# Kernel optimization log

Measured on AMD Instinct MI355X. Metric: run time of the kernel, lower is better.

Reference implementation:

```python
import jax, jax.numpy as jnp
import numpy as np

N, E, D, H, C = 50000, 800000, 64, 2, 64  # nodes, edges, feat, heads, per-head out


def _transformer_conv(x, src, dst, wq, bq, wk, bk, wv, bv, ws, bs):
    n = x.shape[0]
    q = (x @ wq + bq).reshape(n, H, C)
    k = (x @ wk + bk).reshape(n, H, C)
    v = (x @ wv + bv).reshape(n, H, C)
    qi = q[dst]           # [E,H,C] gather at target nodes
    kj = k[src]           # [E,H,C] gather at source nodes
    vj = v[src]
    alpha = jnp.einsum('ehc,ehc->eh', qi, kj) / jnp.sqrt(jnp.asarray(C, x.dtype))
    # segment softmax over incoming edges of each dst node
    amax = jax.ops.segment_max(alpha, dst, num_segments=n)          # [N,H]
    amax = jnp.where(jnp.isfinite(amax), amax, 0.0)
    ex = jnp.exp(alpha - amax[dst])                                  # [E,H]
    denom = jax.ops.segment_sum(ex, dst, num_segments=n)            # [N,H]
    a = ex / (denom[dst] + 1e-16)
    out = jax.ops.segment_sum(a[:, :, None] * vj, dst, num_segments=n)  # [N,H,C]
    out = out.mean(axis=1)                                           # concat=False -> mean heads
    return out + x @ ws + bs                                         # root (skip) connection


def setup_inputs() -> dict:
    key = jax.random.key(0)
    ks = jax.random.split(key, 20)
    x = jax.random.normal(ks[0], (N, D), dtype=jnp.float32)
    edge_index = jax.random.randint(ks[1], (2, E), 0, N, dtype=jnp.int64)
    s = 1.0 / np.sqrt(D)
    def lin(k, din, dout):
        return jax.random.uniform(k, (din, dout), jnp.float32, -s, s)
    inp = {"x": x, "edge_index": edge_index}
    i = 2
    for l, din in ((1, D), (2, C)):
        for nm, dout in (("wq", H * C), ("wk", H * C), ("wv", H * C), ("ws", C)):
            inp[f"l{l}_{nm}"] = lin(ks[i], din, dout); i += 1
            inp[f"l{l}_{nm.replace('w','b')}"] = jnp.zeros((dout,), jnp.float32)
    return inp


def reference(x, edge_index,
              l1_wq, l1_bq, l1_wk, l1_bk, l1_wv, l1_bv, l1_ws, l1_bs,
              l2_wq, l2_bq, l2_wk, l2_bk, l2_wv, l2_bv, l2_ws, l2_bs):
    src, dst = edge_index[0], edge_index[1]
    h = _transformer_conv(x, src, dst, l1_wq, l1_bq, l1_wk, l1_bk, l1_wv, l1_bv, l1_ws, l1_bs)
    h = _transformer_conv(h, src, dst, l2_wq, l2_bq, l2_wk, l2_bk, l2_wv, l2_bv, l2_ws, l2_bs)
    return h
```

## Files before the change

### kernel.cpp

```cpp
#include <hip/hip_runtime.h>
#include <hip/hip_fp16.h>
#include <math.h>


typedef _Float16 half8 __attribute__((ext_vector_type(8)));
typedef _Float16 half4 __attribute__((ext_vector_type(4)));
typedef float floatx4 __attribute__((ext_vector_type(4)));

struct __align__(16) H8 { __half2 a, b, c, d; };
struct __align__(16) F16x8 { _Float16 v[8]; };

static __device__ inline __half2 shfl_xor_h2(__half2 v, int off) {
    union { __half2 h; int i; } u;
    u.h = v;
    u.i = __shfl_xor(u.i, off);
    return u.h;
}

__global__ __launch_bounds__(256) void prep_w_both(
    const float* __restrict__ W0, const float* __restrict__ B0,
    const float* __restrict__ W1, const float* __restrict__ B1,
    const float* __restrict__ W2, const float* __restrict__ B2,
    const float* __restrict__ W3, const float* __restrict__ B3,
    const float* __restrict__ W4, const float* __restrict__ B4,
    const float* __restrict__ W5, const float* __restrict__ B5,
    const float* __restrict__ W6, const float* __restrict__ B6,
    const float* __restrict__ W7, const float* __restrict__ B7,
    _Float16* __restrict__ wht1, _Float16* __restrict__ wht2,
    float* __restrict__ ball1, float* __restrict__ ball2,
    int* __restrict__ counts, int n) {
    const int tid = blockIdx.x * 256 + threadIdx.x;
    const int nt  = gridDim.x * 256;
    for (int idx = tid; idx < 448 * 64; idx += nt) {
        int c = idx >> 6, k = idx & 63;
        float v1, v2;
        if (c < 128)      { v1 = W0[k*128 + c];       v2 = W4[k*128 + c]; }
        else if (c < 256) { v1 = W1[k*128 + (c-128)]; v2 = W5[k*128 + (c-128)]; }
        else if (c < 384) { v1 = W2[k*128 + (c-256)]; v2 = W6[k*128 + (c-256)]; }
        else              { v1 = W3[k*64 + (c-384)];  v2 = W7[k*64 + (c-384)]; }
        wht1[c*64 + k] = (_Float16)v1;
        wht2[c*64 + k] = (_Float16)v2;
        if (k == 0) {
            float b1, b2;
            if (c < 128)      { b1 = B0[c];     b2 = B4[c]; }
            else if (c < 256) { b1 = B1[c-128]; b2 = B5[c-128]; }
            else if (c < 384) { b1 = B2[c-256]; b2 = B6[c-256]; }
            else              { b1 = B3[c-384]; b2 = B7[c-384]; }
            ball1[c] = b1;
            ball2[c] = b2;
        }
    }
    for (int i = tid; i < n; i += nt) counts[i] = 0;
}

__global__ __launch_bounds__(256) void hist_kernel(const int* __restrict__ dst,
                                                   int* __restrict__ counts, int e) {
    int i = blockIdx.x * 256 + threadIdx.x;
    if (i < e) atomicAdd(&counts[dst[i]], 1);
}

__global__ __launch_bounds__(256) void partial_kernel(const int* __restrict__ counts,
                                                      int* __restrict__ partials, int n) {
    int idx = blockIdx.x * 256 + threadIdx.x;
    int v = (idx < n) ? counts[idx] : 0;
    for (int off = 1; off < 64; off <<= 1) v += __shfl_xor(v, off);
    __shared__ int ws[4];
    int wid = threadIdx.x >> 6;
    if ((threadIdx.x & 63) == 0) ws[wid] = v;
    __syncthreads();
    if (threadIdx.x == 0) partials[blockIdx.x] = ws[0] + ws[1] + ws[2] + ws[3];
}

__global__ __launch_bounds__(256) void scanp_kernel(const int* __restrict__ partials,
                                                    int* __restrict__ blockbase, int nb) {
    __shared__ int s[256];
    int t = threadIdx.x;
    int v = (t < nb) ? partials[t] : 0;
    s[t] = v;
    __syncthreads();
    for (int off = 1; off < 256; off <<= 1) {
        int u = (t >= off) ? s[t - off] : 0;
        __syncthreads();
        s[t] += u;
        __syncthreads();
    }
    if (t < nb) blockbase[t] = s[t] - v;
}

__global__ __launch_bounds__(256) void final_kernel(const int* __restrict__ counts,
                                                    const int* __restrict__ blockbase,
                                                    int* __restrict__ offsets,
                                                    int* __restrict__ cursor,
                                                    int n, int total) {
    __shared__ int s[256];
    int t = threadIdx.x;
    int idx = blockIdx.x * 256 + t;
    int v = (idx < n) ? counts[idx] : 0;
    s[t] = v;
    __syncthreads();
    for (int off = 1; off < 256; off <<= 1) {
        int u = (t >= off) ? s[t - off] : 0;
        __syncthreads();
        s[t] += u;
        __syncthreads();
    }
    if (idx < n) {
        int ex = blockbase[blockIdx.x] + s[t] - v;
        offsets[idx] = ex;
        cursor[idx]  = ex;
    }
    if (idx == 0) offsets[n] = total;
}

__global__ __launch_bounds__(256) void scatter_kernel(const int* __restrict__ src,
                                                      const int* __restrict__ dst,
                                                      int* __restrict__ cursor,
                                                      int* __restrict__ ssrc, int e) {
    int i = blockIdx.x * 256 + threadIdx.x;
    if (i < e) {
        int pos = atomicAdd(&cursor[dst[i]], 1);
        ssrc[pos] = src[i];
    }
}

template <int F32IN>
__global__ __launch_bounds__(256) void gemm_mfma(
    const void* __restrict__ Xin, int rows,
    const _Float16* __restrict__ WhT,
    const float* __restrict__ Ball,
    _Float16* __restrict__ Qo,
    _Float16* __restrict__ KVo,
    float* __restrict__ So) {
    const int lane = threadIdx.x & 63;
    const int w    = threadIdx.x >> 6;
    const int kg   = lane >> 4;
    const int li   = lane & 15;
    const int rbase = blockIdx.x * 64 + w * 16;
    const int row  = rbase + li;
    const int crow = row < rows ? row : rows - 1;

    half8 a0, a1;
    if constexpr (F32IN) {
        const float* xp = (const float*)Xin + (size_t)crow * 64 + kg * 8;
        float4 f0 = *(const float4*)xp;
        float4 f1 = *(const float4*)(xp + 4);
        float4 f2 = *(const float4*)(xp + 32);
        float4 f3 = *(const float4*)(xp + 36);
        a0 = half8{(_Float16)f0.x, (_Float16)f0.y, (_Float16)f0.z, (_Float16)f0.w,
                   (_Float16)f1.x, (_Float16)f1.y, (_Float16)f1.z, (_Float16)f1.w};
        a1 = half8{(_Float16)f2.x, (_Float16)f2.y, (_Float16)f2.z, (_Float16)f2.w,
                   (_Float16)f3.x, (_Float16)f3.y, (_Float16)f3.z, (_Float16)f3.w};
    } else {
        const _Float16* xp = (const _Float16*)Xin + (size_t)crow * 64 + kg * 8;
        a0 = *(const half8*)xp;
        a1 = *(const half8*)(xp + 32);
    }

#pragma unroll
    for (int t = 0; t < 28; ++t) {
        const _Float16* wp = WhT + (size_t)(t * 16 + li) * 64 + kg * 8;
        half8 b0 = *(const half8*)wp;
        half8 b1 = *(const half8*)(wp + 32);
        floatx4 acc = {0.f, 0.f, 0.f, 0.f};
        acc = __builtin_amdgcn_mfma_f32_16x16x32_f16(b0, a0, acc, 0, 0, 0);
        acc = __builtin_amdgcn_mfma_f32_16x16x32_f16(b1, a1, acc, 0, 0, 0);
        const int c0 = t * 16 + kg * 4;
        float4 bias = *(const float4*)(Ball + c0);
        if (row < rows) {
            float o0 = acc[0] + bias.x, o1 = acc[1] + bias.y;
            float o2 = acc[2] + bias.z, o3 = acc[3] + bias.w;
            if (t < 8) {
                *(half4*)(Qo + (size_t)row * 128 + c0) =
                    half4{(_Float16)o0, (_Float16)o1, (_Float16)o2, (_Float16)o3};
            } else if (t < 24) {
                *(half4*)(KVo + (size_t)row * 256 + (c0 - 128)) =
                    half4{(_Float16)o0, (_Float16)o1, (_Float16)o2, (_Float16)o3};
            } else {
                *(float4*)(So + (size_t)row * 64 + (c0 - 384)) =
                    make_float4(o0, o1, o2, o3);
            }
        }
    }
}

template <int HALF_OUT>
__global__ __launch_bounds__(256) void attn_kernel(
    const _Float16* __restrict__ Qh,
    const _Float16* __restrict__ KV,
    const int* __restrict__ offs, const int* __restrict__ ssrc,
    const float* __restrict__ skip,
    float* __restrict__ outF, _Float16* __restrict__ outH, int n) {
    int node = (blockIdx.x * 256 + threadIdx.x) >> 6;
    int lane = threadIdx.x & 63;
    if (node >= n) return;
    const int slot = lane >> 4;
    const int koff = ((lane >> 3) & 1) * 64 + (lane & 7) * 8;

    H8 q = *(const H8*)(Qh + (size_t)node * 128 + koff);

    const int beg = offs[node], end = offs[node + 1];
    float m = -INFINITY, l = 0.f;
    __half2 hz = __float2half2_rn(0.f);
    __half2 ha = hz, hb = hz, hc = hz, hd = hz;

    int i = beg;
    bool b0 = false, b1 = false;
    H8 k0, k1, v0, v1;
    if (i < end) {
        int e0 = i + slot, e1 = i + 4 + slot;
        b0 = e0 < end; b1 = e1 < end;
        int s0 = ssrc[b0 ? e0 : end - 1];
        int s1 = ssrc[b1 ? e1 : end - 1];
        const _Float16* p0 = KV + (size_t)s0 * 256 + koff;
        const _Float16* p1 = KV + (size_t)s1 * 256 + koff;
        k0 = *(const H8*)p0; v0 = *(const H8*)(p0 + 128);
        k1 = *(const H8*)p1; v1 = *(const H8*)(p1 + 128);
    }

    while (i < end) {
        const int inext = i + 8;
        bool nb0 = false, nb1 = false;
        H8 nk0, nk1, nv0, nv1;
        if (inext < end) {
            int e0 = inext + slot, e1 = inext + 4 + slot;
            nb0 = e0 < end; nb1 = e1 < end;
            int s0 = ssrc[nb0 ? e0 : end - 1];
            int s1 = ssrc[nb1 ? e1 : end - 1];
            const _Float16* p0 = KV + (size_t)s0 * 256 + koff;
            const _Float16* p1 = KV + (size_t)s1 * 256 + koff;
            nk0 = *(const H8*)p0; nv0 = *(const H8*)(p0 + 128);
            nk1 = *(const H8*)p1; nv1 = *(const H8*)(p1 + 128);
        }

        __half2 dh0 = __hfma2(q.a, k0.a, __hfma2(q.b, k0.b, __hfma2(q.c, k0.c, __hmul2(q.d, k0.d))));
        __half2 dh1 = __hfma2(q.a, k1.a, __hfma2(q.b, k1.b, __hfma2(q.c, k1.c, __hmul2(q.d, k1.d))));
        __half2 pd = __halves2half2(__hadd(dh0.x, dh0.y), __hadd(dh1.x, dh1.y));
        pd = __hadd2(pd, shfl_xor_h2(pd, 1));
        pd = __hadd2(pd, shfl_xor_h2(pd, 2));
        pd = __hadd2(pd, shfl_xor_h2(pd, 4));
        float d0 = b0 ? __half2float(pd.x) * 0.125f : -INFINITY;
        float d1 = b1 ? __half2float(pd.y) * 0.125f : -INFINITY;

        float mx = fmaxf(fmaxf(d0, d1), m);
        float sc = (m == -INFINITY) ? 0.f : __expf(m - mx);
        float p0e = b0 ? __expf(d0 - mx) : 0.f;
        float p1e = b1 ? __expf(d1 - mx) : 0.f;
        l = fmaf(l, sc, p0e + p1e);

        __half2 hsc = __float2half2_rn(sc);
        __half2 hp0 = __float2half2_rn(p0e);
        __half2 hp1 = __float2half2_rn(p1e);
        ha = __hfma2(hp0, v0.a, __hfma2(hp1, v1.a, __hmul2(ha, hsc)));
        hb = __hfma2(hp0, v0.b, __hfma2(hp1, v1.b, __hmul2(hb, hsc)));
        hc = __hfma2(hp0, v0.c, __hfma2(hp1, v1.c, __hmul2(hc, hsc)));
        hd = __hfma2(hp0, v0.d, __hfma2(hp1, v1.d, __hmul2(hd, hsc)));
        m = mx;

        i = inext;
        b0 = nb0; b1 = nb1;
        k0 = nk0; k1 = nk1; v0 = nv0; v1 = nv1;
    }

    float acc[8];
    {
        float2 t0 = __half22float2(ha), t1 = __half22float2(hb);
        float2 t2 = __half22float2(hc), t3 = __half22float2(hd);
        acc[0] = t0.x; acc[1] = t0.y; acc[2] = t1.x; acc[3] = t1.y;
        acc[4] = t2.x; acc[5] = t2.y; acc[6] = t3.x; acc[7] = t3.y;
    }

#pragma unroll
    for (int off = 16; off <= 32; off <<= 1) {
        float mo = __shfl_xor(m, off);
        float lo = __shfl_xor(l, off);
        float ao[8];
#pragma unroll
        for (int j = 0; j < 8; ++j) ao[j] = __shfl_xor(acc[j], off);
        float mm = fmaxf(m, mo);
        float sa = (m  == -INFINITY) ? 0.f : __expf(m  - mm);
        float sb = (mo == -INFINITY) ? 0.f : __expf(mo - mm);
        l = l * sa + lo * sb;
#pragma unroll
        for (int j = 0; j < 8; ++j) acc[j] = acc[j] * sa + ao[j] * sb;
        m = mm;
    }
    float inv = 1.f / (l + 1e-16f);
    float r[8];
#pragma unroll
    for (int j = 0; j < 8; ++j) r[j] = acc[j] * inv;
#pragma unroll
    for (int j = 0; j < 8; ++j) r[j] = 0.5f * (r[j] + __shfl_xor(r[j], 8));

    if (lane < 8) {
        const float4* sp = (const float4*)(skip + (size_t)node * 64 + lane * 8);
        float4 s0 = sp[0], s1 = sp[1];
        float o[8] = {s0.x + r[0], s0.y + r[1], s0.z + r[2], s0.w + r[3],
                      s1.x + r[4], s1.y + r[5], s1.z + r[6], s1.w + r[7]};
        if (HALF_OUT) {
            F16x8 h;
#pragma unroll
            for (int j = 0; j < 8; ++j) h.v[j] = (_Float16)o[j];
            *(F16x8*)(outH + (size_t)node * 64 + lane * 8) = h;
        } else {
            float4* op = (float4*)(outF + (size_t)node * 64 + lane * 8);
            op[0] = make_float4(o[0], o[1], o[2], o[3]);
            op[1] = make_float4(o[4], o[5], o[6], o[7]);
        }
    }
}

extern "C" void kernel_launch(void* const* d_in, const int* in_sizes, int n_in,
                              void* d_out, int out_size, void* d_ws, size_t ws_size,
                              hipStream_t stream) {
    const float* x  = (const float*)d_in[0];
    const int*   ei = (const int*)d_in[1];
    const int N = in_sizes[0] / 64;
    const int E = in_sizes[1] / 2;

    const float* w[16];
    for (int i = 0; i < 16; ++i) w[i] = (const float*)d_in[2 + i];

    char* base = (char*)d_ws;
    size_t off = 0;
    auto alloc = [&](size_t bytes) {
        void* p = base + off;
        off = (off + bytes + 255) & ~(size_t)255;
        return p;
    };
    _Float16* qh   = (_Float16*)alloc((size_t)N * 128 * 2);
    _Float16* kv   = (_Float16*)alloc((size_t)N * 256 * 2);
    float*    sk1  = (float*)alloc((size_t)N * 64 * 4);
    _Float16* h1h  = (_Float16*)alloc((size_t)N * 64 * 2);
    _Float16* wht1 = (_Float16*)alloc(448 * 64 * 2);
    _Float16* wht2 = (_Float16*)alloc(448 * 64 * 2);
    float*    ball1 = (float*)alloc(448 * 4);
    float*    ball2 = (float*)alloc(448 * 4);
    int* counts    = (int*)alloc((size_t)N * 4);
    int* offsets   = (int*)alloc((size_t)(N + 1) * 4);
    int* cursor    = (int*)alloc((size_t)N * 4);
    int* ssrc      = (int*)alloc((size_t)E * 4);
    int* partials  = (int*)alloc(1024 * 4);
    int* blockbase = (int*)alloc(1024 * 4);

    prep_w_both<<<224, 256, 0, stream>>>(
        w[0], w[1], w[2], w[3], w[4], w[5], w[6], w[7],
        w[8], w[9], w[10], w[11], w[12], w[13], w[14], w[15],
        wht1, wht2, ball1, ball2, counts, N);

    int eb = (E + 255) / 256;
    int nb = (N + 255) / 256;
    hist_kernel<<<eb, 256, 0, stream>>>(ei + E, counts, E);
    partial_kernel<<<nb, 256, 0, stream>>>(counts, partials, N);
    scanp_kernel<<<1, 256, 0, stream>>>(partials, blockbase, nb);
    final_kernel<<<nb, 256, 0, stream>>>(counts, blockbase, offsets, cursor, N, E);
    scatter_kernel<<<eb, 256, 0, stream>>>(ei, ei + E, cursor, ssrc, E);

    const int gb = (N + 63) / 64;
    const int ab = (N * 64 + 255) / 256;

    gemm_mfma<1><<<gb, 256, 0, stream>>>(x, N, wht1, ball1, qh, kv, sk1);
    attn_kernel<1><<<ab, 256, 0, stream>>>(qh, kv, offsets, ssrc, sk1,
                                           nullptr, h1h, N);
    gemm_mfma<0><<<gb, 256, 0, stream>>>(h1h, N, wht2, ball2, qh, kv, (float*)d_out);
    attn_kernel<0><<<ab, 256, 0, stream>>>(qh, kv, offsets, ssrc, (float*)d_out,
                                           (float*)d_out, nullptr, N);
}
```

Baseline: 281.0 us.

## Fuse CSR build and first-layer GEMM into one cooperative kernel

Replaces the chain of weight prep, histogram, partial sums, scans, scatter and the layer-1 GEMM with a single cooperative kernel of 1024 blocks that uses grid-wide syncs between phases. The layer-1 GEMM tiles run in the same phase as the degree histogram so the two overlap. The aim is to remove several kernel launch gaps and tail effects from small kernels. The old multi-kernel path is kept as a fallback if the cooperative launch fails. In exchange it adds grid.sync costs and depends on 1024 blocks being co-resident.

```diff
diff --git a/kernel.cpp b/kernel.cpp
--- a/kernel.cpp
+++ b/kernel.cpp
@@ -1,5 +1,6 @@
 #include <hip/hip_runtime.h>
 #include <hip/hip_fp16.h>
+#include <hip/hip_cooperative_groups.h>
 #include <math.h>
 
 
@@ -17,125 +18,17 @@
     return u.h;
 }
 
-__global__ __launch_bounds__(256) void prep_w_both(
-    const float* __restrict__ W0, const float* __restrict__ B0,
-    const float* __restrict__ W1, const float* __restrict__ B1,
-    const float* __restrict__ W2, const float* __restrict__ B2,
-    const float* __restrict__ W3, const float* __restrict__ B3,
-    const float* __restrict__ W4, const float* __restrict__ B4,
-    const float* __restrict__ W5, const float* __restrict__ B5,
-    const float* __restrict__ W6, const float* __restrict__ B6,
-    const float* __restrict__ W7, const float* __restrict__ B7,
-    _Float16* __restrict__ wht1, _Float16* __restrict__ wht2,
-    float* __restrict__ ball1, float* __restrict__ ball2,
-    int* __restrict__ counts, int n) {
-    const int tid = blockIdx.x * 256 + threadIdx.x;
-    const int nt  = gridDim.x * 256;
-    for (int idx = tid; idx < 448 * 64; idx += nt) {
-        int c = idx >> 6, k = idx & 63;
-        float v1, v2;
-        if (c < 128)      { v1 = W0[k*128 + c];       v2 = W4[k*128 + c]; }
-        else if (c < 256) { v1 = W1[k*128 + (c-128)]; v2 = W5[k*128 + (c-128)]; }
-        else if (c < 384) { v1 = W2[k*128 + (c-256)]; v2 = W6[k*128 + (c-256)]; }
-        else              { v1 = W3[k*64 + (c-384)];  v2 = W7[k*64 + (c-384)]; }
-        wht1[c*64 + k] = (_Float16)v1;
-        wht2[c*64 + k] = (_Float16)v2;
-        if (k == 0) {
-            float b1, b2;
-            if (c < 128)      { b1 = B0[c];     b2 = B4[c]; }
-            else if (c < 256) { b1 = B1[c-128]; b2 = B5[c-128]; }
-            else if (c < 384) { b1 = B2[c-256]; b2 = B6[c-256]; }
-            else              { b1 = B3[c-384]; b2 = B7[c-384]; }
-            ball1[c] = b1;
-            ball2[c] = b2;
-        }
-    }
-    for (int i = tid; i < n; i += nt) counts[i] = 0;
-}
-
-__global__ __launch_bounds__(256) void hist_kernel(const int* __restrict__ dst,
-                                                   int* __restrict__ counts, int e) {
-    int i = blockIdx.x * 256 + threadIdx.x;
-    if (i < e) atomicAdd(&counts[dst[i]], 1);
-}
-
-__global__ __launch_bounds__(256) void partial_kernel(const int* __restrict__ counts,
-                                                      int* __restrict__ partials, int n) {
-    int idx = blockIdx.x * 256 + threadIdx.x;
-    int v = (idx < n) ? counts[idx] : 0;
-    for (int off = 1; off < 64; off <<= 1) v += __shfl_xor(v, off);
-    __shared__ int ws[4];
-    int wid = threadIdx.x >> 6;
-    if ((threadIdx.x & 63) == 0) ws[wid] = v;
-    __syncthreads();
-    if (threadIdx.x == 0) partials[blockIdx.x] = ws[0] + ws[1] + ws[2] + ws[3];
-}
-
-__global__ __launch_bounds__(256) void scanp_kernel(const int* __restrict__ partials,
-                                                    int* __restrict__ blockbase, int nb) {
-    __shared__ int s[256];
-    int t = threadIdx.x;
-    int v = (t < nb) ? partials[t] : 0;
-    s[t] = v;
-    __syncthreads();
-    for (int off = 1; off < 256; off <<= 1) {
-        int u = (t >= off) ? s[t - off] : 0;
-        __syncthreads();
-        s[t] += u;
-        __syncthreads();
-    }
-    if (t < nb) blockbase[t] = s[t] - v;
-}
-
-__global__ __launch_bounds__(256) void final_kernel(const int* __restrict__ counts,
-                                                    const int* __restrict__ blockbase,
-                                                    int* __restrict__ offsets,
-                                                    int* __restrict__ cursor,
-                                                    int n, int total) {
-    __shared__ int s[256];
-    int t = threadIdx.x;
-    int idx = blockIdx.x * 256 + t;
-    int v = (idx < n) ? counts[idx] : 0;
-    s[t] = v;
-    __syncthreads();
-    for (int off = 1; off < 256; off <<= 1) {
-        int u = (t >= off) ? s[t - off] : 0;
-        __syncthreads();
-        s[t] += u;
-        __syncthreads();
-    }
-    if (idx < n) {
-        int ex = blockbase[blockIdx.x] + s[t] - v;
-        offsets[idx] = ex;
-        cursor[idx]  = ex;
-    }
-    if (idx == 0) offsets[n] = total;
-}
-
-__global__ __launch_bounds__(256) void scatter_kernel(const int* __restrict__ src,
-                                                      const int* __restrict__ dst,
-                                                      int* __restrict__ cursor,
-                                                      int* __restrict__ ssrc, int e) {
-    int i = blockIdx.x * 256 + threadIdx.x;
-    if (i < e) {
-        int pos = atomicAdd(&cursor[dst[i]], 1);
-        ssrc[pos] = src[i];
-    }
-}
-
 template <int F32IN>
-__global__ __launch_bounds__(256) void gemm_mfma(
+static __device__ __forceinline__ void gemm_tile_body(
     const void* __restrict__ Xin, int rows,
-    const _Float16* __restrict__ WhT,
-    const float* __restrict__ Ball,
-    _Float16* __restrict__ Qo,
-    _Float16* __restrict__ KVo,
-    float* __restrict__ So) {
-    const int lane = threadIdx.x & 63;
-    const int w    = threadIdx.x >> 6;
+    const _Float16* __restrict__ WhT, const float* __restrict__ Ball,
+    _Float16* __restrict__ Qo, _Float16* __restrict__ KVo,
+    float* __restrict__ So, int blk, int tix) {
+    const int lane = tix & 63;
+    const int w    = tix >> 6;
     const int kg   = lane >> 4;
     const int li   = lane & 15;
-    const int rbase = blockIdx.x * 64 + w * 16;
+    const int rbase = blk * 64 + w * 16;
     const int row  = rbase + li;
     const int crow = row < rows ? row : rows - 1;
 
@@ -183,6 +76,229 @@
     }
 }
 
+static __device__ __forceinline__ void prep_body(
+    const float* const* W, _Float16* wht1, _Float16* wht2,
+    float* ball1, float* ball2, int* counts, int n, int tid, int nt) {
+    for (int idx = tid; idx < 448 * 64; idx += nt) {
+        int c = idx >> 6, k = idx & 63;
+        float v1, v2;
+        if (c < 128)      { v1 = W[0][k*128 + c];        v2 = W[8][k*128 + c]; }
+        else if (c < 256) { v1 = W[2][k*128 + (c-128)];  v2 = W[10][k*128 + (c-128)]; }
+        else if (c < 384) { v1 = W[4][k*128 + (c-256)];  v2 = W[12][k*128 + (c-256)]; }
+        else              { v1 = W[6][k*64 + (c-384)];   v2 = W[14][k*64 + (c-384)]; }
+        wht1[c*64 + k] = (_Float16)v1;
+        wht2[c*64 + k] = (_Float16)v2;
+        if (k == 0) {
+            float b1, b2;
+            if (c < 128)      { b1 = W[1][c];       b2 = W[9][c]; }
+            else if (c < 256) { b1 = W[3][c-128];   b2 = W[11][c-128]; }
+            else if (c < 384) { b1 = W[5][c-256];   b2 = W[13][c-256]; }
+            else              { b1 = W[7][c-384];   b2 = W[15][c-384]; }
+            ball1[c] = b1;
+            ball2[c] = b2;
+        }
+    }
+    for (int i = tid; i < n; i += nt) counts[i] = 0;
+}
+
+struct SetupArgs {
+    const float* W[16];
+    const float* x;
+    const int* ei;
+    int* counts;
+    int* offsets;
+    int* cursor;
+    int* ssrc;
+    int* partials;
+    int* blockbase;
+    _Float16* wht1;
+    _Float16* wht2;
+    float* ball1;
+    float* ball2;
+    _Float16* qh;
+    _Float16* kv;
+    float* sk1;
+    int N, E;
+};
+
+__global__ __launch_bounds__(256, 4) void setup_coop(SetupArgs a) {
+    namespace cg = cooperative_groups;
+    cg::grid_group grid = cg::this_grid();
+    const int tid = blockIdx.x * 256 + threadIdx.x;
+    const int nt  = gridDim.x * 256;
+    __shared__ int sh[256];
+    __shared__ int ws[4];
+
+    prep_body(a.W, a.wht1, a.wht2, a.ball1, a.ball2, a.counts, a.N, tid, nt);
+    grid.sync();
+
+    {
+        const int ntile = (a.N + 63) >> 6;
+        for (int tb = blockIdx.x; tb < ntile; tb += gridDim.x)
+            gemm_tile_body<1>(a.x, a.N, a.wht1, a.ball1, a.qh, a.kv, a.sk1,
+                              tb, threadIdx.x);
+        const int* dst = a.ei + a.E;
+        for (int i = tid; i < a.E; i += nt) atomicAdd(&a.counts[dst[i]], 1);
+    }
+    grid.sync();
+
+    const int nch = (a.N + 255) >> 8;
+    for (int b = blockIdx.x; b < nch; b += gridDim.x) {
+        int idx = b * 256 + threadIdx.x;
+        int v = (idx < a.N) ? a.counts[idx] : 0;
+        for (int off = 1; off < 64; off <<= 1) v += __shfl_xor(v, off);
+        if ((threadIdx.x & 63) == 0) ws[threadIdx.x >> 6] = v;
+        __syncthreads();
+        if (threadIdx.x == 0)
+            a.partials[b] = ws[0] + ws[1] + ws[2] + ws[3];
+        __syncthreads();
+    }
+    grid.sync();
+
+    if (blockIdx.x == 0) {
+        int t = threadIdx.x;
+        int v = (t < nch) ? a.partials[t] : 0;
+        sh[t] = v;
+        __syncthreads();
+        for (int off = 1; off < 256; off <<= 1) {
+            int u = (t >= off) ? sh[t - off] : 0;
+            __syncthreads();
+            sh[t] += u;
+            __syncthreads();
+        }
+        if (t < nch) a.blockbase[t] = sh[t] - v;
+    }
+    grid.sync();
+
+    for (int b = blockIdx.x; b < nch; b += gridDim.x) {
+        int t = threadIdx.x;
+        int idx = b * 256 + t;
+        int v = (idx < a.N) ? a.counts[idx] : 0;
+        sh[t] = v;
+        __syncthreads();
+        for (int off = 1; off < 256; off <<= 1) {
+            int u = (t >= off) ? sh[t - off] : 0;
+            __syncthreads();
+            sh[t] += u;
+            __syncthreads();
+        }
+        if (idx < a.N) {
+            int ex = a.blockbase[b] + sh[t] - v;
+            a.offsets[idx] = ex;
+            a.cursor[idx]  = ex;
+        }
+        if (idx == 0) a.offsets[a.N] = a.E;
+        __syncthreads();
+    }
+    grid.sync();
+
+    {
+        const int* dst = a.ei + a.E;
+        const int* srcp = a.ei;
+        for (int i = tid; i < a.E; i += nt) {
+            int pos = atomicAdd(&a.cursor[dst[i]], 1);
+            a.ssrc[pos] = srcp[i];
+        }
+    }
+}
+
+__global__ __launch_bounds__(256) void prep_w_both(
+    const float* __restrict__ W0, const float* __restrict__ B0,
+    const float* __restrict__ W1, const float* __restrict__ B1,
+    const float* __restrict__ W2, const float* __restrict__ B2,
+    const float* __restrict__ W3, const float* __restrict__ B3,
+    const float* __restrict__ W4, const float* __restrict__ B4,
+    const float* __restrict__ W5, const float* __restrict__ B5,
+    const float* __restrict__ W6, const float* __restrict__ B6,
+    const float* __restrict__ W7, const float* __restrict__ B7,
+    _Float16* __restrict__ wht1, _Float16* __restrict__ wht2,
+    float* __restrict__ ball1, float* __restrict__ ball2,
+    int* __restrict__ counts, int n) {
+    const float* W[16] = {W0,B0,W1,B1,W2,B2,W3,B3,W4,B4,W5,B5,W6,B6,W7,B7};
+    prep_body(W, wht1, wht2, ball1, ball2, counts, n,
+              blockIdx.x * 256 + threadIdx.x, gridDim.x * 256);
+}
+
+__global__ __launch_bounds__(256) void hist_kernel(const int* __restrict__ dst,
+                                                   int* __restrict__ counts, int e) {
+    int i = blockIdx.x * 256 + threadIdx.x;
+    if (i < e) atomicAdd(&counts[dst[i]], 1);
+}
+
+__global__ __launch_bounds__(256) void partial_kernel(const int* __restrict__ counts,
+                                                      int* __restrict__ partials, int n) {
+    int idx = blockIdx.x * 256 + threadIdx.x;
+    int v = (idx < n) ? counts[idx] : 0;
+    for (int off = 1; off < 64; off <<= 1) v += __shfl_xor(v, off);
+    __shared__ int ws[4];
+    int wid = threadIdx.x >> 6;
+    if ((threadIdx.x & 63) == 0) ws[wid] = v;
+    __syncthreads();
+    if (threadIdx.x == 0) partials[blockIdx.x] = ws[0] + ws[1] + ws[2] + ws[3];
+}
+
+__global__ __launch_bounds__(256) void scanp_kernel(const int* __restrict__ partials,
+                                                    int* __restrict__ blockbase, int nb) {
+    __shared__ int s[256];
+    int t = threadIdx.x;
+    int v = (t < nb) ? partials[t] : 0;
+    s[t] = v;
+    __syncthreads();
+    for (int off = 1; off < 256; off <<= 1) {
+        int u = (t >= off) ? s[t - off] : 0;
+        __syncthreads();
+        s[t] += u;
+        __syncthreads();
+    }
+    if (t < nb) blockbase[t] = s[t] - v;
+}
+
+__global__ __launch_bounds__(256) void final_kernel(const int* __restrict__ counts,
+                                                    const int* __restrict__ blockbase,
+                                                    int* __restrict__ offsets,
+                                                    int* __restrict__ cursor,
+                                                    int n, int total) {
+    __shared__ int s[256];
+    int t = threadIdx.x;
+    int idx = blockIdx.x * 256 + t;
+    int v = (idx < n) ? counts[idx] : 0;
+    s[t] = v;
+    __syncthreads();
+    for (int off = 1; off < 256; off <<= 1) {
+        int u = (t >= off) ? s[t - off] : 0;
+        __syncthreads();
+        s[t] += u;
+        __syncthreads();
+    }
+    if (idx < n) {
+        int ex = blockbase[blockIdx.x] + s[t] - v;
+        offsets[idx] = ex;
+        cursor[idx]  = ex;
+    }
+    if (idx == 0) offsets[n] = total;
+}
+
+__global__ __launch_bounds__(256) void scatter_kernel(const int* __restrict__ src,
+                                                      const int* __restrict__ dst,
+                                                      int* __restrict__ cursor,
+                                                      int* __restrict__ ssrc, int e) {
+    int i = blockIdx.x * 256 + threadIdx.x;
+    if (i < e) {
+        int pos = atomicAdd(&cursor[dst[i]], 1);
+        ssrc[pos] = src[i];
+    }
+}
+
+template <int F32IN>
+__global__ __launch_bounds__(256) void gemm_mfma(
+    const void* __restrict__ Xin, int rows,
+    const _Float16* __restrict__ WhT, const float* __restrict__ Ball,
+    _Float16* __restrict__ Qo, _Float16* __restrict__ KVo,
+    float* __restrict__ So) {
+    gemm_tile_body<F32IN>(Xin, rows, WhT, Ball, Qo, KVo, So,
+                          blockIdx.x, threadIdx.x);
+}
+
 template <int HALF_OUT>
 __global__ __launch_bounds__(256) void attn_kernel(
     const _Float16* __restrict__ Qh,
@@ -342,23 +458,37 @@
     int* partials  = (int*)alloc(1024 * 4);
     int* blockbase = (int*)alloc(1024 * 4);
 
-    prep_w_both<<<224, 256, 0, stream>>>(
-        w[0], w[1], w[2], w[3], w[4], w[5], w[6], w[7],
-        w[8], w[9], w[10], w[11], w[12], w[13], w[14], w[15],
-        wht1, wht2, ball1, ball2, counts, N);
-
-    int eb = (E + 255) / 256;
-    int nb = (N + 255) / 256;
-    hist_kernel<<<eb, 256, 0, stream>>>(ei + E, counts, E);
-    partial_kernel<<<nb, 256, 0, stream>>>(counts, partials, N);
-    scanp_kernel<<<1, 256, 0, stream>>>(partials, blockbase, nb);
-    final_kernel<<<nb, 256, 0, stream>>>(counts, blockbase, offsets, cursor, N, E);
-    scatter_kernel<<<eb, 256, 0, stream>>>(ei, ei + E, cursor, ssrc, E);
+    SetupArgs sa;
+    for (int i = 0; i < 16; ++i) sa.W[i] = w[i];
+    sa.x = x; sa.ei = ei;
+    sa.counts = counts; sa.offsets = offsets; sa.cursor = cursor; sa.ssrc = ssrc;
+    sa.partials = partials; sa.blockbase = blockbase;
+    sa.wht1 = wht1; sa.wht2 = wht2; sa.ball1 = ball1; sa.ball2 = ball2;
+    sa.qh = qh; sa.kv = kv; sa.sk1 = sk1;
+    sa.N = N; sa.E = E;
+
+    void* kargs[] = { &sa };
+    hipError_t cerr = hipLaunchCooperativeKernel(
+        (const void*)setup_coop, dim3(1024), dim3(256), kargs, 0, stream);
 
     const int gb = (N + 63) / 64;
     const int ab = (N * 64 + 255) / 256;
 
-    gemm_mfma<1><<<gb, 256, 0, stream>>>(x, N, wht1, ball1, qh, kv, sk1);
+    if (cerr != hipSuccess) {
+        int eb = (E + 255) / 256;
+        int nb = (N + 255) / 256;
+        prep_w_both<<<224, 256, 0, stream>>>(
+            w[0], w[1], w[2], w[3], w[4], w[5], w[6], w[7],
+            w[8], w[9], w[10], w[11], w[12], w[13], w[14], w[15],
+            wht1, wht2, ball1, ball2, counts, N);
+        hist_kernel<<<eb, 256, 0, stream>>>(ei + E, counts, E);
+        partial_kernel<<<nb, 256, 0, stream>>>(counts, partials, N);
+        scanp_kernel<<<1, 256, 0, stream>>>(partials, blockbase, nb);
+        final_kernel<<<nb, 256, 0, stream>>>(counts, blockbase, offsets, cursor, N, E);
+        scatter_kernel<<<eb, 256, 0, stream>>>(ei, ei + E, cursor, ssrc, E);
+        gemm_mfma<1><<<gb, 256, 0, stream>>>(x, N, wht1, ball1, qh, kv, sk1);
+    }
+
     attn_kernel<1><<<ab, 256, 0, stream>>>(qh, kv, offsets, ssrc, sk1,
                                            nullptr, h1h, N);
     gemm_mfma<0><<<gb, 256, 0, stream>>>(h1h, N, wht2, ball2, qh, kv, (float*)d_out);
```

New measurement: 862.4 us. 207% more time.

## Replace three-kernel scan with decoupled lookback scan and tile GEMM over more rows

Applied to the files above, without the earlier changes.

Replaces the partial/scan/final three-launch exclusive scan with a single-pass decoupled lookback scan, using a 64-bit state array that prep_w_both zeroes. This removes two kernel launches and the extra pass over counts. The GEMM now has each wave process four 16-row tiles so every weight fragment load is reused across 64 rows, which cuts redundant weight traffic. The lookback assumes blocks are scheduled in forward order and spin-waits on predecessors. The GEMM change raises register use and leaves fewer blocks in the grid.

```diff
diff --git a/kernel.cpp b/kernel.cpp
--- a/kernel.cpp
+++ b/kernel.cpp
@@ -28,7 +28,7 @@
     const float* __restrict__ W7, const float* __restrict__ B7,
     _Float16* __restrict__ wht1, _Float16* __restrict__ wht2,
     float* __restrict__ ball1, float* __restrict__ ball2,
-    int* __restrict__ counts, int n) {
+    int* __restrict__ counts, unsigned long long* __restrict__ state, int n) {
     const int tid = blockIdx.x * 256 + threadIdx.x;
     const int nt  = gridDim.x * 256;
     for (int idx = tid; idx < 448 * 64; idx += nt) {
@@ -51,6 +51,7 @@
         }
     }
     for (int i = tid; i < n; i += nt) counts[i] = 0;
+    if (tid < 256) state[tid] = 0ull;
 }
 
 __global__ __launch_bounds__(256) void hist_kernel(const int* __restrict__ dst,
@@ -59,23 +60,14 @@
     if (i < e) atomicAdd(&counts[dst[i]], 1);
 }
 
-__global__ __launch_bounds__(256) void partial_kernel(const int* __restrict__ counts,
-                                                      int* __restrict__ partials, int n) {
-    int idx = blockIdx.x * 256 + threadIdx.x;
+__global__ __launch_bounds__(256) void scan_lookback(
+    const int* __restrict__ counts, unsigned long long* __restrict__ state,
+    int* __restrict__ offsets, int* __restrict__ cursor, int n, int total) {
+    const int b = blockIdx.x, t = threadIdx.x;
+    const int idx = b * 256 + t;
     int v = (idx < n) ? counts[idx] : 0;
-    for (int off = 1; off < 64; off <<= 1) v += __shfl_xor(v, off);
-    __shared__ int ws[4];
-    int wid = threadIdx.x >> 6;
-    if ((threadIdx.x & 63) == 0) ws[wid] = v;
-    __syncthreads();
-    if (threadIdx.x == 0) partials[blockIdx.x] = ws[0] + ws[1] + ws[2] + ws[3];
-}
-
-__global__ __launch_bounds__(256) void scanp_kernel(const int* __restrict__ partials,
-                                                    int* __restrict__ blockbase, int nb) {
     __shared__ int s[256];
-    int t = threadIdx.x;
-    int v = (t < nb) ? partials[t] : 0;
+    __shared__ int exs;
     s[t] = v;
     __syncthreads();
     for (int off = 1; off < 256; off <<= 1) {
@@ -84,30 +76,39 @@
         s[t] += u;
         __syncthreads();
     }
-    if (t < nb) blockbase[t] = s[t] - v;
-}
-
-__global__ __launch_bounds__(256) void final_kernel(const int* __restrict__ counts,
-                                                    const int* __restrict__ blockbase,
-                                                    int* __restrict__ offsets,
-                                                    int* __restrict__ cursor,
-                                                    int n, int total) {
-    __shared__ int s[256];
-    int t = threadIdx.x;
-    int idx = blockIdx.x * 256 + t;
-    int v = (idx < n) ? counts[idx] : 0;
-    s[t] = v;
+    const int incl = s[t];
+    const int aggregate = s[255];
+    if (t == 0) {
+        if (b == 0) {
+            __hip_atomic_store(&state[0],
+                (2ull << 32) | (unsigned)aggregate,
+                __ATOMIC_RELEASE, __HIP_MEMORY_SCOPE_AGENT);
+            exs = 0;
+        } else {
+            __hip_atomic_store(&state[b],
+                (1ull << 32) | (unsigned)aggregate,
+                __ATOMIC_RELEASE, __HIP_MEMORY_SCOPE_AGENT);
+            int ex = 0;
+            int p = b - 1;
+            while (p >= 0) {
+                unsigned long long st = __hip_atomic_load(&state[p],
+                    __ATOMIC_ACQUIRE, __HIP_MEMORY_SCOPE_AGENT);
+                unsigned tag = (unsigned)(st >> 32);
+                if (tag == 2u) { ex += (int)(unsigned)st; break; }
+                if (tag == 1u) { ex += (int)(unsigned)st; --p; }
+            }
+            __hip_atomic_store(&state[b],
+                (2ull << 32) | (unsigned)(ex + aggregate),
+                __ATOMIC_RELEASE, __HIP_MEMORY_SCOPE_AGENT);
+            exs = ex;
+        }
+    }
     __syncthreads();
-    for (int off = 1; off < 256; off <<= 1) {
-        int u = (t >= off) ? s[t - off] : 0;
-        __syncthreads();
-        s[t] += u;
-        __syncthreads();
-    }
+    const int ex = exs;
     if (idx < n) {
-        int ex = blockbase[blockIdx.x] + s[t] - v;
-        offsets[idx] = ex;
-        cursor[idx]  = ex;
+        int e0 = ex + incl - v;
+        offsets[idx] = e0;
+        cursor[idx]  = e0;
     }
     if (idx == 0) offsets[n] = total;
 }
@@ -135,25 +136,30 @@
     const int w    = threadIdx.x >> 6;
     const int kg   = lane >> 4;
     const int li   = lane & 15;
-    const int rbase = blockIdx.x * 64 + w * 16;
-    const int row  = rbase + li;
-    const int crow = row < rows ? row : rows - 1;
-
-    half8 a0, a1;
-    if constexpr (F32IN) {
-        const float* xp = (const float*)Xin + (size_t)crow * 64 + kg * 8;
-        float4 f0 = *(const float4*)xp;
-        float4 f1 = *(const float4*)(xp + 4);
-        float4 f2 = *(const float4*)(xp + 32);
-        float4 f3 = *(const float4*)(xp + 36);
-        a0 = half8{(_Float16)f0.x, (_Float16)f0.y, (_Float16)f0.z, (_Float16)f0.w,
-                   (_Float16)f1.x, (_Float16)f1.y, (_Float16)f1.z, (_Float16)f1.w};
-        a1 = half8{(_Float16)f2.x, (_Float16)f2.y, (_Float16)f2.z, (_Float16)f2.w,
-                   (_Float16)f3.x, (_Float16)f3.y, (_Float16)f3.z, (_Float16)f3.w};
-    } else {
-        const _Float16* xp = (const _Float16*)Xin + (size_t)crow * 64 + kg * 8;
-        a0 = *(const half8*)xp;
-        a1 = *(const half8*)(xp + 32);
+    const int rbase = blockIdx.x * 256 + w * 64;
+
+    half8 a0[4], a1[4];
+    int rowr[4];
+#pragma unroll
+    for (int rt = 0; rt < 4; ++rt) {
+        int row = rbase + rt * 16 + li;
+        rowr[rt] = row;
+        int crow = row < rows ? row : rows - 1;
+        if constexpr (F32IN) {
+            const float* xp = (const float*)Xin + (size_t)crow * 64 + kg * 8;
+            float4 f0 = *(const float4*)xp;
+            float4 f1 = *(const float4*)(xp + 4);
+            float4 f2 = *(const float4*)(xp + 32);
+            float4 f3 = *(const float4*)(xp + 36);
+            a0[rt] = half8{(_Float16)f0.x, (_Float16)f0.y, (_Float16)f0.z, (_Float16)f0.w,
+                           (_Float16)f1.x, (_Float16)f1.y, (_Float16)f1.z, (_Float16)f1.w};
+            a1[rt] = half8{(_Float16)f2.x, (_Float16)f2.y, (_Float16)f2.z, (_Float16)f2.w,
+                           (_Float16)f3.x, (_Float16)f3.y, (_Float16)f3.z, (_Float16)f3.w};
+        } else {
+            const _Float16* xp = (const _Float16*)Xin + (size_t)crow * 64 + kg * 8;
+            a0[rt] = *(const half8*)xp;
+            a1[rt] = *(const half8*)(xp + 32);
+        }
     }
 
 #pragma unroll
@@ -161,23 +167,27 @@
         const _Float16* wp = WhT + (size_t)(t * 16 + li) * 64 + kg * 8;
         half8 b0 = *(const half8*)wp;
         half8 b1 = *(const half8*)(wp + 32);
-        floatx4 acc = {0.f, 0.f, 0.f, 0.f};
-        acc = __builtin_amdgcn_mfma_f32_16x16x32_f16(b0, a0, acc, 0, 0, 0);
-        acc = __builtin_amdgcn_mfma_f32_16x16x32_f16(b1, a1, acc, 0, 0, 0);
         const int c0 = t * 16 + kg * 4;
         float4 bias = *(const float4*)(Ball + c0);
-        if (row < rows) {
-            float o0 = acc[0] + bias.x, o1 = acc[1] + bias.y;
-            float o2 = acc[2] + bias.z, o3 = acc[3] + bias.w;
-            if (t < 8) {
-                *(half4*)(Qo + (size_t)row * 128 + c0) =
-                    half4{(_Float16)o0, (_Float16)o1, (_Float16)o2, (_Float16)o3};
-            } else if (t < 24) {
-                *(half4*)(KVo + (size_t)row * 256 + (c0 - 128)) =
-                    half4{(_Float16)o0, (_Float16)o1, (_Float16)o2, (_Float16)o3};
-            } else {
-                *(float4*)(So + (size_t)row * 64 + (c0 - 384)) =
-                    make_float4(o0, o1, o2, o3);
+#pragma unroll
+        for (int rt = 0; rt < 4; ++rt) {
+            floatx4 acc = {0.f, 0.f, 0.f, 0.f};
+            acc = __builtin_amdgcn_mfma_f32_16x16x32_f16(b0, a0[rt], acc, 0, 0, 0);
+            acc = __builtin_amdgcn_mfma_f32_16x16x32_f16(b1, a1[rt], acc, 0, 0, 0);
+            const int row = rowr[rt];
+            if (row < rows) {
+                float o0 = acc[0] + bias.x, o1 = acc[1] + bias.y;
+                float o2 = acc[2] + bias.z, o3 = acc[3] + bias.w;
+                if (t < 8) {
+                    *(half4*)(Qo + (size_t)row * 128 + c0) =
+                        half4{(_Float16)o0, (_Float16)o1, (_Float16)o2, (_Float16)o3};
+                } else if (t < 24) {
+                    *(half4*)(KVo + (size_t)row * 256 + (c0 - 128)) =
+                        half4{(_Float16)o0, (_Float16)o1, (_Float16)o2, (_Float16)o3};
+                } else {
+                    *(float4*)(So + (size_t)row * 64 + (c0 - 384)) =
+                        make_float4(o0, o1, o2, o3);
+                }
             }
         }
     }
@@ -339,23 +349,20 @@
     int* offsets   = (int*)alloc((size_t)(N + 1) * 4);
     int* cursor    = (int*)alloc((size_t)N * 4);
     int* ssrc      = (int*)alloc((size_t)E * 4);
-    int* partials  = (int*)alloc(1024 * 4);
-    int* blockbase = (int*)alloc(1024 * 4);
+    unsigned long long* state = (unsigned long long*)alloc(256 * 8);
 
     prep_w_both<<<224, 256, 0, stream>>>(
         w[0], w[1], w[2], w[3], w[4], w[5], w[6], w[7],
         w[8], w[9], w[10], w[11], w[12], w[13], w[14], w[15],
-        wht1, wht2, ball1, ball2, counts, N);
+        wht1, wht2, ball1, ball2, counts, state, N);
 
     int eb = (E + 255) / 256;
     int nb = (N + 255) / 256;
     hist_kernel<<<eb, 256, 0, stream>>>(ei + E, counts, E);
-    partial_kernel<<<nb, 256, 0, stream>>>(counts, partials, N);
-    scanp_kernel<<<1, 256, 0, stream>>>(partials, blockbase, nb);
-    final_kernel<<<nb, 256, 0, stream>>>(counts, blockbase, offsets, cursor, N, E);
+    scan_lookback<<<nb, 256, 0, stream>>>(counts, state, offsets, cursor, N, E);
     scatter_kernel<<<eb, 256, 0, stream>>>(ei, ei + E, cursor, ssrc, E);
 
-    const int gb = (N + 63) / 64;
+    const int gb = (N + 255) / 256;
     const int ab = (N * 64 + 255) / 256;
 
     gemm_mfma<1><<<gb, 256, 0, stream>>>(x, N, wht1, ball1, qh, kv, sk1);
```

Measured after the change: 315.6 us. +12.3%, slower.

## Fuse histogram into first GEMM and replace three-pass scan with atomic allocation

Applied to the files above, without the earlier changes.

Merges the dst-degree histogram into the layer-1 GEMM launch as extra blocks, so both run concurrently in one kernel. It also replaces the partial/scan/final three-kernel prefix sum with a single kernel that takes per-wavefront bases from a global atomic counter. Segments are no longer laid out in node order, so attention reads the end as offset plus count. This removes four kernel launches and their serialization. The cost is a non-contiguous, nondeterministic CSR layout and atomic contention on one counter.

```diff
diff --git a/kernel.cpp b/kernel.cpp
--- a/kernel.cpp
+++ b/kernel.cpp
@@ -28,7 +28,7 @@
     const float* __restrict__ W7, const float* __restrict__ B7,
     _Float16* __restrict__ wht1, _Float16* __restrict__ wht2,
     float* __restrict__ ball1, float* __restrict__ ball2,
-    int* __restrict__ counts, int n) {
+    int* __restrict__ counts, int* __restrict__ gcounter, int n) {
     const int tid = blockIdx.x * 256 + threadIdx.x;
     const int nt  = gridDim.x * 256;
     for (int idx = tid; idx < 448 * 64; idx += nt) {
@@ -51,91 +51,20 @@
         }
     }
     for (int i = tid; i < n; i += nt) counts[i] = 0;
-}
-
-__global__ __launch_bounds__(256) void hist_kernel(const int* __restrict__ dst,
-                                                   int* __restrict__ counts, int e) {
-    int i = blockIdx.x * 256 + threadIdx.x;
-    if (i < e) atomicAdd(&counts[dst[i]], 1);
-}
-
-__global__ __launch_bounds__(256) void partial_kernel(const int* __restrict__ counts,
-                                                      int* __restrict__ partials, int n) {
-    int idx = blockIdx.x * 256 + threadIdx.x;
-    int v = (idx < n) ? counts[idx] : 0;
-    for (int off = 1; off < 64; off <<= 1) v += __shfl_xor(v, off);
-    __shared__ int ws[4];
-    int wid = threadIdx.x >> 6;
-    if ((threadIdx.x & 63) == 0) ws[wid] = v;
-    __syncthreads();
-    if (threadIdx.x == 0) partials[blockIdx.x] = ws[0] + ws[1] + ws[2] + ws[3];
-}
-
-__global__ __launch_bounds__(256) void scanp_kernel(const int* __restrict__ partials,
-                                                    int* __restrict__ blockbase, int nb) {
-    __shared__ int s[256];
-    int t = threadIdx.x;
-    int v = (t < nb) ? partials[t] : 0;
-    s[t] = v;
-    __syncthreads();
-    for (int off = 1; off < 256; off <<= 1) {
-        int u = (t >= off) ? s[t - off] : 0;
-        __syncthreads();
-        s[t] += u;
-        __syncthreads();
-    }
-    if (t < nb) blockbase[t] = s[t] - v;
-}
-
-__global__ __launch_bounds__(256) void final_kernel(const int* __restrict__ counts,
-                                                    const int* __restrict__ blockbase,
-                                                    int* __restrict__ offsets,
-                                                    int* __restrict__ cursor,
-                                                    int n, int total) {
-    __shared__ int s[256];
-    int t = threadIdx.x;
-    int idx = blockIdx.x * 256 + t;
-    int v = (idx < n) ? counts[idx] : 0;
-    s[t] = v;
-    __syncthreads();
-    for (int off = 1; off < 256; off <<= 1) {
-        int u = (t >= off) ? s[t - off] : 0;
-        __syncthreads();
-        s[t] += u;
-        __syncthreads();
-    }
-    if (idx < n) {
-        int ex = blockbase[blockIdx.x] + s[t] - v;
-        offsets[idx] = ex;
-        cursor[idx]  = ex;
-    }
-    if (idx == 0) offsets[n] = total;
-}
-
-__global__ __launch_bounds__(256) void scatter_kernel(const int* __restrict__ src,
-                                                      const int* __restrict__ dst,
-                                                      int* __restrict__ cursor,
-                                                      int* __restrict__ ssrc, int e) {
-    int i = blockIdx.x * 256 + threadIdx.x;
-    if (i < e) {
-        int pos = atomicAdd(&cursor[dst[i]], 1);
-        ssrc[pos] = src[i];
-    }
+    if (tid == 0) *gcounter = 0;
 }
 
 template <int F32IN>
-__global__ __launch_bounds__(256) void gemm_mfma(
+static __device__ __forceinline__ void gemm_tile_body(
     const void* __restrict__ Xin, int rows,
-    const _Float16* __restrict__ WhT,
-    const float* __restrict__ Ball,
-    _Float16* __restrict__ Qo,
-    _Float16* __restrict__ KVo,
-    float* __restrict__ So) {
-    const int lane = threadIdx.x & 63;
-    const int w    = threadIdx.x >> 6;
+    const _Float16* __restrict__ WhT, const float* __restrict__ Ball,
+    _Float16* __restrict__ Qo, _Float16* __restrict__ KVo,
+    float* __restrict__ So, int blk, int tix) {
+    const int lane = tix & 63;
+    const int w    = tix >> 6;
     const int kg   = lane >> 4;
     const int li   = lane & 15;
-    const int rbase = blockIdx.x * 64 + w * 16;
+    const int rbase = blk * 64 + w * 16;
     const int row  = rbase + li;
     const int crow = row < rows ? row : rows - 1;
 
@@ -183,11 +112,71 @@
     }
 }
 
+__global__ __launch_bounds__(256) void gemm1_hist(
+    const float* __restrict__ X, int rows,
+    const _Float16* __restrict__ WhT, const float* __restrict__ Ball,
+    _Float16* __restrict__ Qo, _Float16* __restrict__ KVo,
+    float* __restrict__ So,
+    const int* __restrict__ dst, int* __restrict__ counts, int e, int gb) {
+    if ((int)blockIdx.x < gb) {
+        gemm_tile_body<1>(X, rows, WhT, Ball, Qo, KVo, So,
+                          blockIdx.x, threadIdx.x);
+    } else {
+        int i = ((int)blockIdx.x - gb) * 256 + threadIdx.x;
+        if (i < e) atomicAdd(&counts[dst[i]], 1);
+    }
+}
+
+__global__ __launch_bounds__(256) void alloc_kernel(
+    const int* __restrict__ counts, int* __restrict__ gcounter,
+    int* __restrict__ offsets, int* __restrict__ cursor, int n) {
+    int idx = blockIdx.x * 256 + threadIdx.x;
+    int lane = threadIdx.x & 63;
+    int v = (idx < n) ? counts[idx] : 0;
+    int pre = v;
+#pragma unroll
+    for (int off = 1; off < 64; off <<= 1) {
+        int u = __shfl_up(pre, off);
+        if (lane >= off) pre += u;
+    }
+    int wtot = __shfl(pre, 63);
+    int base = 0;
+    if (lane == 63) base = atomicAdd(gcounter, wtot);
+    base = __shfl(base, 63);
+    if (idx < n) {
+        int ex = base + pre - v;
+        offsets[idx] = ex;
+        cursor[idx]  = ex;
+    }
+}
+
+__global__ __launch_bounds__(256) void scatter_kernel(const int* __restrict__ src,
+                                                      const int* __restrict__ dst,
+                                                      int* __restrict__ cursor,
+                                                      int* __restrict__ ssrc, int e) {
+    int i = blockIdx.x * 256 + threadIdx.x;
+    if (i < e) {
+        int pos = atomicAdd(&cursor[dst[i]], 1);
+        ssrc[pos] = src[i];
+    }
+}
+
+template <int F32IN>
+__global__ __launch_bounds__(256) void gemm_mfma(
+    const void* __restrict__ Xin, int rows,
+    const _Float16* __restrict__ WhT, const float* __restrict__ Ball,
+    _Float16* __restrict__ Qo, _Float16* __restrict__ KVo,
+    float* __restrict__ So) {
+    gemm_tile_body<F32IN>(Xin, rows, WhT, Ball, Qo, KVo, So,
+                          blockIdx.x, threadIdx.x);
+}
+
 template <int HALF_OUT>
 __global__ __launch_bounds__(256) void attn_kernel(
     const _Float16* __restrict__ Qh,
     const _Float16* __restrict__ KV,
-    const int* __restrict__ offs, const int* __restrict__ ssrc,
+    const int* __restrict__ offs, const int* __restrict__ cnts,
+    const int* __restrict__ ssrc,
     const float* __restrict__ skip,
     float* __restrict__ outF, _Float16* __restrict__ outH, int n) {
     int node = (blockIdx.x * 256 + threadIdx.x) >> 6;
@@ -198,7 +187,8 @@
 
     H8 q = *(const H8*)(Qh + (size_t)node * 128 + koff);
 
-    const int beg = offs[node], end = offs[node + 1];
+    const int beg = offs[node];
+    const int end = beg + cnts[node];
     float m = -INFINITY, l = 0.f;
     __half2 hz = __float2half2_rn(0.f);
     __half2 ha = hz, hb = hz, hc = hz, hd = hz;
@@ -339,29 +329,26 @@
     int* offsets   = (int*)alloc((size_t)(N + 1) * 4);
     int* cursor    = (int*)alloc((size_t)N * 4);
     int* ssrc      = (int*)alloc((size_t)E * 4);
-    int* partials  = (int*)alloc(1024 * 4);
-    int* blockbase = (int*)alloc(1024 * 4);
+    int* gcounter  = (int*)alloc(256 * 4);
 
     prep_w_both<<<224, 256, 0, stream>>>(
         w[0], w[1], w[2], w[3], w[4], w[5], w[6], w[7],
         w[8], w[9], w[10], w[11], w[12], w[13], w[14], w[15],
-        wht1, wht2, ball1, ball2, counts, N);
-
-    int eb = (E + 255) / 256;
-    int nb = (N + 255) / 256;
-    hist_kernel<<<eb, 256, 0, stream>>>(ei + E, counts, E);
-    partial_kernel<<<nb, 256, 0, stream>>>(counts, partials, N);
-    scanp_kernel<<<1, 256, 0, stream>>>(partials, blockbase, nb);
-    final_kernel<<<nb, 256, 0, stream>>>(counts, blockbase, offsets, cursor, N, E);
-    scatter_kernel<<<eb, 256, 0, stream>>>(ei, ei + E, cursor, ssrc, E);
-
+        wht1, wht2, ball1, ball2, counts, gcounter, N);
+
+    const int eb = (E + 255) / 256;
+    const int nb = (N + 255) / 256;
     const int gb = (N + 63) / 64;
     const int ab = (N * 64 + 255) / 256;
 
-    gemm_mfma<1><<<gb, 256, 0, stream>>>(x, N, wht1, ball1, qh, kv, sk1);
-    attn_kernel<1><<<ab, 256, 0, stream>>>(qh, kv, offsets, ssrc, sk1,
+    gemm1_hist<<<gb + eb, 256, 0, stream>>>(x, N, wht1, ball1, qh, kv, sk1,
+                                            ei + E, counts, E, gb);
+    alloc_kernel<<<nb, 256, 0, stream>>>(counts, gcounter, offsets, cursor, N);
+    scatter_kernel<<<eb, 256, 0, stream>>>(ei, ei + E, cursor, ssrc, E);
+
+    attn_kernel<1><<<ab, 256, 0, stream>>>(qh, kv, offsets, counts, ssrc, sk1,
                                            nullptr, h1h, N);
     gemm_mfma<0><<<gb, 256, 0, stream>>>(h1h, N, wht2, ball2, qh, kv, (float*)d_out);
-    attn_kernel<0><<<ab, 256, 0, stream>>>(qh, kv, offsets, ssrc, (float*)d_out,
+    attn_kernel<0><<<ab, 256, 0, stream>>>(qh, kv, offsets, counts, ssrc, (float*)d_out,
                                            (float*)d_out, nullptr, N);
 }
```

Result: no change. 278.3 us (-1.0%).
